# Optimization experiments

Hardware: AMD Instinct MI355X
Metric: run time of the kernel (lower is better)

Reference implementation:

```python
import jax, jax.numpy as jnp
import numpy as np

T, B, IN, H, E = 1024, 64, 64, 512, 128


def _gru_layer(x, Wih, Whh, bih, bhh):
    # x: [T, B, D_in]; Wih: [3H, D_in]; Whh: [3H, H]; PyTorch gate order: r, z, n
    gx = jnp.einsum('tbi,gi->tbg', x, Wih) + bih  # [T, B, 3H]

    def step(h, gx_t):
        gh = h @ Whh.T + bhh
        xr, xz, xn = jnp.split(gx_t, 3, axis=-1)
        hr, hz, hn = jnp.split(gh, 3, axis=-1)
        r = jax.nn.sigmoid(xr + hr)
        z = jax.nn.sigmoid(xz + hz)
        n = jnp.tanh(xn + r * hn)
        h_new = (1.0 - z) * n + z * h
        return h_new, h_new

    h0 = jnp.zeros((x.shape[1], Whh.shape[1]), x.dtype)
    _, ys = jax.lax.scan(step, h0, gx)
    return ys  # [T, B, H]


def setup_inputs() -> dict:
    key = jax.random.key(0)
    ks = iter(jax.random.split(key, 32))
    s = 0.05
    d = {'x': jax.random.normal(next(ks), (T, B, IN), jnp.float32)}
    # encoder GRU: layer0 IN->H, layer1 H->H; linear H->E
    d['e_Wih0'] = jax.random.normal(next(ks), (3 * H, IN), jnp.float32) * s
    d['e_Whh0'] = jax.random.normal(next(ks), (3 * H, H), jnp.float32) * s
    d['e_bih0'] = jax.random.normal(next(ks), (3 * H,), jnp.float32) * s
    d['e_bhh0'] = jax.random.normal(next(ks), (3 * H,), jnp.float32) * s
    d['e_Wih1'] = jax.random.normal(next(ks), (3 * H, H), jnp.float32) * s
    d['e_Whh1'] = jax.random.normal(next(ks), (3 * H, H), jnp.float32) * s
    d['e_bih1'] = jax.random.normal(next(ks), (3 * H,), jnp.float32) * s
    d['e_bhh1'] = jax.random.normal(next(ks), (3 * H,), jnp.float32) * s
    d['e_lW'] = jax.random.normal(next(ks), (E, H), jnp.float32) * s
    d['e_lb'] = jax.random.normal(next(ks), (E,), jnp.float32) * s
    # decoder GRU: layer0 E->H, layer1 H->H; linear H->IN
    d['d_Wih0'] = jax.random.normal(next(ks), (3 * H, E), jnp.float32) * s
    d['d_Whh0'] = jax.random.normal(next(ks), (3 * H, H), jnp.float32) * s
    d['d_bih0'] = jax.random.normal(next(ks), (3 * H,), jnp.float32) * s
    d['d_bhh0'] = jax.random.normal(next(ks), (3 * H,), jnp.float32) * s
    d['d_Wih1'] = jax.random.normal(next(ks), (3 * H, H), jnp.float32) * s
    d['d_Whh1'] = jax.random.normal(next(ks), (3 * H, H), jnp.float32) * s
    d['d_bih1'] = jax.random.normal(next(ks), (3 * H,), jnp.float32) * s
    d['d_bhh1'] = jax.random.normal(next(ks), (3 * H,), jnp.float32) * s
    d['d_lW'] = jax.random.normal(next(ks), (IN, H), jnp.float32) * s
    d['d_lb'] = jax.random.normal(next(ks), (IN,), jnp.float32) * s
    return d


def reference(x, e_Wih0, e_Whh0, e_bih0, e_bhh0, e_Wih1, e_Whh1, e_bih1, e_bhh1, e_lW, e_lb,
              d_Wih0, d_Whh0, d_bih0, d_bhh0, d_Wih1, d_Whh1, d_bih1, d_bhh1, d_lW, d_lb):
    # encoder
    h = _gru_layer(x, e_Wih0, e_Whh0, e_bih0, e_bhh0)
    h = _gru_layer(h, e_Wih1, e_Whh1, e_bih1, e_bhh1)
    z = jnp.einsum('tbh,eh->tbe', h, e_lW) + e_lb  # [T, B, E]
    # repeat last timestep embedding across time
    z_rep = jnp.broadcast_to(z[-1][None], (x.shape[0],) + z.shape[1:])
    # decoder
    g = _gru_layer(z_rep, d_Wih0, d_Whh0, d_bih0, d_bhh0)
    g = _gru_layer(g, d_Wih1, d_Whh1, d_bih1, d_bhh1)
    out = jnp.einsum('tbh,ih->tbi', g, d_lW) + d_lb  # [T, B, IN]
    return out
```

## Files before the change

kernel.cpp:

```cpp
#include <hip/hip_runtime.h>


#define SC_AGT __HIP_MEMORY_SCOPE_AGENT

typedef _Float16 half8 __attribute__((ext_vector_type(8)));
typedef float floatx4 __attribute__((ext_vector_type(4)));

union H8 { unsigned long long q[2]; half8 h; uint4 u4; };
union HU { _Float16 f; unsigned short u; };

static constexpr size_t OFF_FLAGS = 0;
static constexpr size_t OFF_GEP   = 16384;
static constexpr size_t OFF_Z     = 16448;
static constexpr size_t OFF_GXC   = OFF_Z + 64 * 128 * 4;
static constexpr size_t OFF_H0    = OFF_GXC + 64 * 1536 * 4;
static constexpr size_t OFF_H1    = OFF_H0 + 2 * 64 * 512 * 2;
static constexpr size_t OFF_G0    = OFF_H1 + 2 * 64 * 512 * 2;
static constexpr size_t OFF_G1    = OFF_G0 + 2 * 64 * 512 * 2;
static constexpr size_t OFF_LWP   = OFF_G1 + 2 * 64 * 512 * 2;
static constexpr size_t OFF_WF    = OFF_LWP + 64 * 512 * 2;

static constexpr int E_PREP    = 1;
static constexpr int E_ENC_BEG = 2;
static constexpr int E_ENC_END = 1026;
static constexpr int E_Z       = 1027;
static constexpr int E_GXC     = 1028;
static constexpr int E_DEC_BEG = 1029;
static constexpr int E_LAST    = 2054;

__device__ __forceinline__ unsigned long long ald64(const void* p) {
  return __hip_atomic_load((const unsigned long long*)p, __ATOMIC_RELAXED, SC_AGT);
}
__device__ __forceinline__ int ald32(const int* p) {
  return __hip_atomic_load(p, __ATOMIC_RELAXED, SC_AGT);
}
__device__ __forceinline__ void ast16(void* p, unsigned short v) {
  __hip_atomic_store((unsigned short*)p, v, __ATOMIC_RELAXED, SC_AGT);
}
__device__ __forceinline__ void ast32u(void* p, unsigned int v) {
  __hip_atomic_store((unsigned int*)p, v, __ATOMIC_RELAXED, SC_AGT);
}
__device__ __forceinline__ void astf(float* p, float v) {
  __hip_atomic_store(p, v, __ATOMIC_RELAXED, SC_AGT);
}

__device__ __forceinline__ float sigm(float x) { return 1.f / (1.f + __expf(-x)); }
__device__ __forceinline__ float tanh_f(float x) {
  x = fminf(fmaxf(x, -30.f), 30.f);
  const float e2 = __expf(2.f * x);
  return (e2 - 1.f) / (e2 + 1.f);
}

#define MFMA(a, b, c) __builtin_amdgcn_mfma_f32_16x16x32_f16((a), (b), (c), 0, 0, 0)

__device__ __forceinline__ void pollwait(const int* flags, int target) {
  const int lane = threadIdx.x & 63;
  for (;;) {
    const int v0 = ald32(flags + (size_t)lane * 16);
    const int v1 = ald32(flags + (size_t)(64 + lane) * 16);
    const int v2 = ald32(flags + (size_t)(128 + lane) * 16);
    const int v3 = ald32(flags + (size_t)(192 + lane) * 16);
    const bool ok = (v0 >= target) && (v1 >= target) && (v2 >= target) &&
                    (v3 >= target);
    if (__ballot(ok) == ~0ull) break;
    __builtin_amdgcn_s_sleep(2);
  }
  asm volatile("" ::: "memory");
}

__device__ __forceinline__ void pollwait_gep(const int* gep, int target) {
  for (;;) {
    if (ald32(gep) >= target) break;
    __builtin_amdgcn_s_sleep(1);
  }
  asm volatile("" ::: "memory");
}

__device__ __forceinline__ void tick_partials(
    const char* __restrict__ wf,
    int g0u, int g1u, int g2u, int g3u,
    int nk0, int nk1, int nk2, int nk3,
    int kc0, int kccnt, int hsplit,
    const float* __restrict__ xs,
    const _Float16* __restrict__ ax,
    const _Float16* __restrict__ ah,
    bool hvalid, int hcb, int lane,
    float* __restrict__ partsW) {
  const int quad = lane >> 4;
  H8 A[8];
#pragma unroll
  for (int c = 0; c < 8; ++c) {
    A[c].q[0] = 0ull;
    A[c].q[1] = 0ull;
    if (c < kccnt) {
      const int kc = kc0 + c;
      if (kc < hsplit) {
        if (xs) {
          const float* p = xs + kc * 32 + quad * 8;
          const float4 f0 = *(const float4*)p;
          const float4 f1 = *(const float4*)(p + 4);
          H8 t;
          t.h[0] = (_Float16)f0.x; t.h[1] = (_Float16)f0.y;
          t.h[2] = (_Float16)f0.z; t.h[3] = (_Float16)f0.w;
          t.h[4] = (_Float16)f1.x; t.h[5] = (_Float16)f1.y;
          t.h[6] = (_Float16)f1.z; t.h[7] = (_Float16)f1.w;
          A[c] = t;
        } else {
          const _Float16* p = ax + kc * 32 + quad * 8;
          A[c].q[0] = ald64(p);
          A[c].q[1] = ald64(p + 4);
        }
      } else if (hvalid) {
        const _Float16* p = ah + (kc - hsplit) * 32 + quad * 8;
        A[c].q[0] = ald64(p);
        A[c].q[1] = ald64(p + 4);
      }
    }
  }
  floatx4 ar = {0.f, 0.f, 0.f, 0.f};
  floatx4 az = ar, axn = ar, ahn = ar;
  const size_t lb = (size_t)lane * 16;
#pragma unroll
  for (int c = 0; c < 8; ++c) {
    if (c < kccnt) {
      const int kc = kc0 + c;
      const bool inH = (kc >= hsplit);
      if (!inH || hvalid) {
        {
          const char* b = wf + (size_t)(g0u + hcb * nk0 + kc) * 2048 + lb;
          H8 whi;
          whi.u4 = *(const uint4*)b;
          ar = MFMA(A[c].h, whi.h, ar);
        }
        {
          const char* b = wf + (size_t)(g1u + hcb * nk1 + kc) * 2048 + lb;
          H8 whi;
          whi.u4 = *(const uint4*)b;
          az = MFMA(A[c].h, whi.h, az);
        }
        if (!inH) {
          const char* b = wf + (size_t)(g2u + hcb * nk2 + kc) * 2048 + lb;
          H8 whi;
          whi.u4 = *(const uint4*)b;
          axn = MFMA(A[c].h, whi.h, axn);
        } else {
          const char* b = wf + (size_t)(g3u + hcb * nk3 + (kc - hsplit)) * 2048 + lb;
          H8 whi;
          whi.u4 = *(const uint4*)b;
          ahn = MFMA(A[c].h, whi.h, ahn);
        }
      }
    }
  }
  const int m = lane & 15;
#pragma unroll
  for (int i = 0; i < 4; ++i) {
    const int idx = (quad * 4 + i) * 16 + m;
    partsW[0 * 256 + idx] = ar[i];
    partsW[1 * 256 + idx] = az[i];
    partsW[2 * 256 + idx] = axn[i];
    partsW[3 * 256 + idx] = ahn[i];
  }
}

extern "C" __global__ void __launch_bounds__(256, 1) gru_ae_kernel(
    const float* __restrict__ x,
    const float* __restrict__ eW0i, const float* __restrict__ eW0h,
    const float* __restrict__ eb0i, const float* __restrict__ eb0h,
    const float* __restrict__ eW1i, const float* __restrict__ eW1h,
    const float* __restrict__ eb1i, const float* __restrict__ eb1h,
    const float* __restrict__ elW, const float* __restrict__ elb,
    const float* __restrict__ dW0i, const float* __restrict__ dW0h,
    const float* __restrict__ db0i, const float* __restrict__ db0h,
    const float* __restrict__ dW1i, const float* __restrict__ dW1h,
    const float* __restrict__ db1i, const float* __restrict__ db1h,
    const float* __restrict__ dlW, const float* __restrict__ dlb,
    float* __restrict__ out, char* __restrict__ ws) {
  const int tid = threadIdx.x, bid = blockIdx.x;
  const int lane = tid & 63, w = tid >> 6;
  const int quad = lane >> 4, m = lane & 15;
  const bool isP0 = bid < 128;
  const int pb = isP0 ? bid : bid - 128;
  const int rb = pb >> 5, hcb = pb & 31;

  int* flags = (int*)(ws + OFF_FLAGS);
  int* gep = (int*)(ws + OFF_GEP);
  float* zbuf = (float*)(ws + OFF_Z);
  float* gxc = (float*)(ws + OFF_GXC);
  _Float16* h0r = (_Float16*)(ws + OFF_H0);
  _Float16* h1r = (_Float16*)(ws + OFF_H1);
  _Float16* g0r = (_Float16*)(ws + OFF_G0);
  _Float16* g1r = (_Float16*)(ws + OFF_G1);
  _Float16* lWp = (_Float16*)(ws + OFF_LWP);
  const char* wfb = ws + OFF_WF;
  const char* wf0 = wfb;
  const char* wf1 = wfb + (size_t)1728 * 2048;
  const char* wf2 = wfb + (size_t)(1728 + 3072) * 2048;
  const char* wf3 = wfb + (size_t)(1728 + 3072 + 1536) * 2048;

  __shared__ float parts[4][4][256];
  __shared__ float outp[4][64];

  float hold_s = 0.f;
  float br = 0.f, bz = 0.f, bx = 0.f, bh = 0.f;
  float gxr_s = 0.f, gxz_s = 0.f, gxn_s = 0.f;

  for (int e = E_PREP; e <= E_LAST; ++e) {
    if (e > E_PREP) {
      if (w == 0) {
        if (bid == 0) {
          pollwait(flags, e - 1);
          __hip_atomic_store(gep, e - 1, __ATOMIC_RELAXED, SC_AGT);
        } else {
          pollwait_gep(gep, e - 1);
        }
      }
      __syncthreads();
    }

    if (e == E_PREP) {
      const int uend[4] = {1728, 4800, 6336, 9408};
      const int gub_[4][4] = {{0, 576, 1152, 1216}, {0, 1024, 2048, 2560},
                              {0, 512, 1024, 1024}, {0, 1024, 2048, 2560}};
      const int nkc_[4][4] = {{18, 18, 2, 16}, {32, 32, 16, 16},
                              {16, 16, 0, 16}, {32, 32, 16, 16}};
      const size_t wbL[4] = {0, (size_t)1728 * 2048, (size_t)4800 * 2048,
                             (size_t)6336 * 2048};
      const int wgid = bid * 4 + w;
      for (int unit = wgid; unit < 9408; unit += 1024) {
        int L = 0, lu = unit;
        if (unit >= uend[2]) { L = 3; lu = unit - uend[2]; }
        else if (unit >= uend[1]) { L = 2; lu = unit - uend[1]; }
        else if (unit >= uend[0]) { L = 1; lu = unit - uend[0]; }
        int g;
        if (lu < gub_[L][1]) g = 0;
        else if (lu < gub_[L][2]) g = 1;
        else if (nkc_[L][2] > 0 && lu < gub_[L][3]) g = 2;
        else g = 3;
        const int r2 = lu - gub_[L][g];
        const int nk = nkc_[L][g];
        const int hcbp = r2 / nk, kcp = r2 % nk;
        const int colp = hcbp * 16 + m;
        const float *Wi, *Wh;
        int Din;
        if (L == 0)      { Wi = eW0i; Wh = eW0h; Din = 64; }
        else if (L == 1) { Wi = eW1i; Wh = eW1h; Din = 512; }
        else if (L == 2) { Wi = nullptr; Wh = dW0h; Din = 0; }
        else             { Wi = dW1i; Wh = dW1h; Din = 512; }
        char* ub = (char*)(ws + OFF_WF) + wbL[L] + (size_t)lu * 2048 + lane * 16;
#pragma unroll
        for (int jj = 0; jj < 4; ++jj) {
          unsigned int hiw = 0, low = 0;
#pragma unroll
          for (int j2 = 0; j2 < 2; ++j2) {
            const int j = jj * 2 + j2;
            const int k = kcp * 32 + quad * 8 + j;
            float wv;
            if (g <= 1) {
              if (Wi && k < Din) wv = Wi[(size_t)(g * 512 + colp) * Din + k];
              else wv = Wh[(size_t)(g * 512 + colp) * 512 + (k - (Wi ? Din : 0))];
            } else if (g == 2) {
              wv = Wi[(size_t)(1024 + colp) * Din + k];
            } else {
              wv = Wh[(size_t)(1024 + colp) * 512 + k];
            }
            HU hi, lo;
            hi.f = (_Float16)wv;
            lo.f = (_Float16)(wv - (float)hi.f);
            hiw |= ((unsigned int)hi.u) << (16 * j2);
            low |= ((unsigned int)lo.u) << (16 * j2);
          }
          ast32u(ub + jj * 4, hiw);
          ast32u(ub + 1024 + jj * 4, low);
        }
      }
      const int gid = bid * 256 + tid;
      if (gid < 32768) {
        HU cv;
        cv.f = (_Float16)dlW[gid];
        ast16(lWp + gid, cv.u);
      }
    } else if (e <= E_ENC_END) {
      const int u = e - E_ENC_BEG;
      if (e == E_ENC_BEG) {
        const int colg = hcb * 16 + m;
        if (isP0) {
          br = eb0i[colg] + eb0h[colg];
          bz = eb0i[512 + colg] + eb0h[512 + colg];
          bx = eb0i[1024 + colg];
          bh = eb0h[1024 + colg];
        } else {
          br = eb1i[colg] + eb1h[colg];
          bz = eb1i[512 + colg] + eb1h[512 + colg];
          bx = eb1i[1024 + colg];
          bh = eb1h[1024 + colg];
        }
        hold_s = 0.f;
      }
      if (isP0) {
        if (u <= 1023) {
          const int t = u;
          const float* xs = x + ((size_t)t * 64 + rb * 16 + m) * 64;
          const _Float16* ah = h0r + (size_t)((t - 1) & 1) * 32768 + (rb * 16 + m) * 512;
          const int kc0 = (w == 0) ? 0 : (w == 1) ? 5 : (w == 2) ? 10 : 14;
          const int cnt = (w < 2) ? 5 : 4;
          tick_partials(wf0, 0, 576, 1152, 1216, 18, 18, 2, 16, kc0, cnt, 2,
                        xs, nullptr, ah, t >= 1, hcb, lane, &parts[w][0][0]);
        }
      } else {
        if (u >= 1) {
          const int t = u - 1;
          const _Float16* ax = h0r + (size_t)(t & 1) * 32768 + (rb * 16 + m) * 512;
          const _Float16* ah = h1r + (size_t)((t - 1) & 1) * 32768 + (rb * 16 + m) * 512;
          tick_partials(wf1, 0, 1024, 2048, 2560, 32, 32, 16, 16, w * 8, 8, 16,
                        nullptr, ax, ah, t >= 1, hcb, lane, &parts[w][0][0]);
        }
      }
    } else if (e == E_Z) {
      const int b = bid >> 2, e0 = (bid & 3) * 32;
      float acc = 0.f;
      if (lane < 32) {
        const _Float16* hsrc = h1r + (size_t)1 * 32768 + b * 512;
        const float* lwrow = elW + (size_t)(e0 + lane) * 512;
        for (int ch = 0; ch < 16; ++ch) {
          const int k = w * 128 + ch * 8;
          H8 a;
          a.q[0] = ald64(hsrc + k);
          a.q[1] = ald64(hsrc + k + 4);
          const float4 l0 = *(const float4*)(lwrow + k);
          const float4 l1 = *(const float4*)(lwrow + k + 4);
          acc += (float)a.h[0] * l0.x + (float)a.h[1] * l0.y +
                 (float)a.h[2] * l0.z + (float)a.h[3] * l0.w +
                 (float)a.h[4] * l1.x + (float)a.h[5] * l1.y +
                 (float)a.h[6] * l1.z + (float)a.h[7] * l1.w;
        }
      }
      outp[w][lane] = acc;
    } else if (e == E_GXC) {
      const int b = bid & 63, cb = (bid >> 6) * 384;
      for (int idx = w * 64 + lane; idx < 384; idx += 256) {
        const int c = cb + idx;
        float acc = db0i[c];
        const float* zr = zbuf + b * 128;
        const float* wr = dW0i + (size_t)c * 128;
        for (int k = 0; k < 128; ++k) acc += zr[k] * wr[k];
        astf(&gxc[(size_t)b * 1536 + c], acc);
      }
    } else {
      const int v = e - E_DEC_BEG;
      if (e == E_DEC_BEG) {
        const int colg = hcb * 16 + m;
        if (isP0) {
          br = db0h[colg];
          bz = db0h[512 + colg];
          bx = 0.f;
          bh = db0h[1024 + colg];
          const int row0 = rb * 16 + quad * 4 + w;
          gxr_s = gxc[(size_t)row0 * 1536 + colg];
          gxz_s = gxc[(size_t)row0 * 1536 + 512 + colg];
          gxn_s = gxc[(size_t)row0 * 1536 + 1024 + colg];
        } else {
          br = db1i[colg] + db1h[colg];
          bz = db1i[512 + colg] + db1h[512 + colg];
          bx = db1i[1024 + colg];
          bh = db1h[1024 + colg];
        }
        hold_s = 0.f;
      }
      if (isP0) {
        if (v <= 1023) {
          const int t = v;
          const _Float16* ah = g0r + (size_t)((t - 1) & 1) * 32768 + (rb * 16 + m) * 512;
          tick_partials(wf2, 0, 512, 0, 1024, 16, 16, 0, 16, w * 4, 4, 0,
                        nullptr, nullptr, ah, t >= 1, hcb, lane, &parts[w][0][0]);
        }
        if (pb < 64 && v >= 2) {
          const int t2 = v - 2;
          const _Float16* gsrc = g1r + (size_t)(t2 & 1) * 32768 + pb * 512;
          const _Float16* lrow = lWp + (size_t)lane * 512;
          float acc = 0.f;
          for (int ch = 0; ch < 16; ++ch) {
            const int k = w * 128 + ch * 8;
            H8 a, lw;
            a.q[0] = ald64(gsrc + k);
            a.q[1] = ald64(gsrc + k + 4);
            lw.u4 = *(const uint4*)(lrow + k);
#pragma unroll
            for (int j = 0; j < 8; ++j) acc += (float)a.h[j] * (float)lw.h[j];
          }
          outp[w][lane] = acc;
        }
      } else {
        if (v >= 1 && v <= 1024) {
          const int t = v - 1;
          const _Float16* ax = g0r + (size_t)(t & 1) * 32768 + (rb * 16 + m) * 512;
          const _Float16* ah = g1r + (size_t)((t - 1) & 1) * 32768 + (rb * 16 + m) * 512;
          tick_partials(wf3, 0, 1024, 2048, 2560, 32, 32, 16, 16, w * 8, 8, 16,
                        nullptr, ax, ah, t >= 1, hcb, lane, &parts[w][0][0]);
        }
      }
    }

    __syncthreads();

    if (e >= E_ENC_BEG && e <= E_ENC_END) {
      const int u = e - E_ENC_BEG;
      const bool doep = isP0 ? (u <= 1023) : (u >= 1);
      if (doep) {
        const int idx = (quad * 4 + w) * 16 + m;
        const float sr = parts[0][0][idx] + parts[1][0][idx] +
                         parts[2][0][idx] + parts[3][0][idx];
        const float sz = parts[0][1][idx] + parts[1][1][idx] +
                         parts[2][1][idx] + parts[3][1][idx];
        const float sx = parts[0][2][idx] + parts[1][2][idx] +
                         parts[2][2][idx] + parts[3][2][idx];
        const float sh = parts[0][3][idx] + parts[1][3][idx] +
                         parts[2][3][idx] + parts[3][3][idx];
        const float r = sigm(sr + br);
        const float z = sigm(sz + bz);
        const float n = tanh_f(sx + bx + r * (sh + bh));
        const float hh = (1.f - z) * n + z * hold_s;
        hold_s = hh;
        _Float16* ring = isP0 ? (h0r + (size_t)(u & 1) * 32768)
                              : (h1r + (size_t)((u - 1) & 1) * 32768);
        HU cv;
        cv.f = (_Float16)hh;
        ast16(ring + (rb * 16 + quad * 4 + w) * 512 + hcb * 16 + m, cv.u);
      }
    } else if (e == E_Z) {
      if (w == 0 && lane < 32) {
        const int b = bid >> 2, e0 = (bid & 3) * 32;
        const float s = outp[0][lane] + outp[1][lane] + outp[2][lane] +
                        outp[3][lane] + elb[e0 + lane];
        astf(&zbuf[b * 128 + e0 + lane], s);
      }
    } else if (e >= E_DEC_BEG) {
      const int v = e - E_DEC_BEG;
      if (isP0) {
        if (v <= 1023) {
          const int idx = (quad * 4 + w) * 16 + m;
          const float sr = parts[0][0][idx] + parts[1][0][idx] +
                           parts[2][0][idx] + parts[3][0][idx];
          const float sz = parts[0][1][idx] + parts[1][1][idx] +
                           parts[2][1][idx] + parts[3][1][idx];
          const float sh = parts[0][3][idx] + parts[1][3][idx] +
                           parts[2][3][idx] + parts[3][3][idx];
          const float r = sigm(sr + gxr_s + br);
          const float z = sigm(sz + gxz_s + bz);
          const float n = tanh_f(gxn_s + r * (sh + bh));
          const float hh = (1.f - z) * n + z * hold_s;
          hold_s = hh;
          HU cv;
          cv.f = (_Float16)hh;
          ast16(g0r + (size_t)(v & 1) * 32768 +
                    (rb * 16 + quad * 4 + w) * 512 + hcb * 16 + m,
                cv.u);
        }
        if (w == 0 && pb < 64 && v >= 2) {
          const int t2 = v - 2;
          const float s = outp[0][lane] + outp[1][lane] + outp[2][lane] +
                          outp[3][lane] + dlb[lane];
          astf(&out[((size_t)t2 * 64 + pb) * 64 + lane], s);
        }
      } else {
        if (v >= 1 && v <= 1024) {
          const int idx = (quad * 4 + w) * 16 + m;
          const float sr = parts[0][0][idx] + parts[1][0][idx] +
                           parts[2][0][idx] + parts[3][0][idx];
          const float sz = parts[0][1][idx] + parts[1][1][idx] +
                           parts[2][1][idx] + parts[3][1][idx];
          const float sx = parts[0][2][idx] + parts[1][2][idx] +
                           parts[2][2][idx] + parts[3][2][idx];
          const float sh = parts[0][3][idx] + parts[1][3][idx] +
                           parts[2][3][idx] + parts[3][3][idx];
          const float r = sigm(sr + br);
          const float z = sigm(sz + bz);
          const float n = tanh_f(sx + bx + r * (sh + bh));
          const float hh = (1.f - z) * n + z * hold_s;
          hold_s = hh;
          HU cv;
          cv.f = (_Float16)hh;
          ast16(g1r + (size_t)((v - 1) & 1) * 32768 +
                    (rb * 16 + quad * 4 + w) * 512 + hcb * 16 + m,
                cv.u);
        }
      }
    }

    __syncthreads();

    if (tid == 0) {
      __hip_atomic_store(&flags[bid * 16], e, __ATOMIC_RELAXED, SC_AGT);
    }
  }
}

extern "C" void kernel_launch(void* const* d_in, const int* in_sizes, int n_in,
                              void* d_out, int out_size, void* d_ws, size_t ws_size,
                              hipStream_t stream) {
  (void)in_sizes; (void)n_in; (void)out_size; (void)ws_size;
  hipMemsetAsync(d_ws, 0, 16448, stream);
  hipLaunchKernelGGL(gru_ae_kernel, dim3(256), dim3(256), 0, stream,
                     (const float*)d_in[0],
                     (const float*)d_in[1], (const float*)d_in[2],
                     (const float*)d_in[3], (const float*)d_in[4],
                     (const float*)d_in[5], (const float*)d_in[6],
                     (const float*)d_in[7], (const float*)d_in[8],
                     (const float*)d_in[9], (const float*)d_in[10],
                     (const float*)d_in[11], (const float*)d_in[12],
                     (const float*)d_in[13], (const float*)d_in[14],
                     (const float*)d_in[15], (const float*)d_in[16],
                     (const float*)d_in[17], (const float*)d_in[18],
                     (const float*)d_in[19], (const float*)d_in[20],
                     (float*)d_out, (char*)d_ws);
}
```

Baseline: 14.66 ms.

## Replace global per-step barrier with row-group flag waits and 4-deep rings

Per-timestep synchronization no longer waits on a global barrier coordinated by block 0. Each block now polls only the flags of the 64 blocks in its batch-row group across both layers, with a lagged target for producer-side blocks. The hidden-state rings grow from double to quadruple buffering so blocks can drift apart by a few steps without overwriting data still being read. The decoder output projection is reassigned to blocks inside each row group so its dependencies stay local. This removes the global barrier's serialization and latency, but relies on the ring depth and lag targets being correct to avoid races.

Result: slower. 16.03 ms (+9.4%).

```diff
diff --git a/kernel.cpp b/kernel.cpp
--- a/kernel.cpp
+++ b/kernel.cpp
@@ -13,11 +13,12 @@
 static constexpr size_t OFF_GEP   = 16384;
 static constexpr size_t OFF_Z     = 16448;
 static constexpr size_t OFF_GXC   = OFF_Z + 64 * 128 * 4;
+static constexpr size_t RING_SZ   = 4 * 64 * 512 * 2;
 static constexpr size_t OFF_H0    = OFF_GXC + 64 * 1536 * 4;
-static constexpr size_t OFF_H1    = OFF_H0 + 2 * 64 * 512 * 2;
-static constexpr size_t OFF_G0    = OFF_H1 + 2 * 64 * 512 * 2;
-static constexpr size_t OFF_G1    = OFF_G0 + 2 * 64 * 512 * 2;
-static constexpr size_t OFF_LWP   = OFF_G1 + 2 * 64 * 512 * 2;
+static constexpr size_t OFF_H1    = OFF_H0 + RING_SZ;
+static constexpr size_t OFF_G0    = OFF_H1 + RING_SZ;
+static constexpr size_t OFF_G1    = OFF_G0 + RING_SZ;
+static constexpr size_t OFF_LWP   = OFF_G1 + RING_SZ;
 static constexpr size_t OFF_WF    = OFF_LWP + 64 * 512 * 2;
 
 static constexpr int E_PREP    = 1;
@@ -72,6 +73,19 @@
   for (;;) {
     if (ald32(gep) >= target) break;
     __builtin_amdgcn_s_sleep(1);
+  }
+  asm volatile("" ::: "memory");
+}
+
+__device__ __forceinline__ void pollwait_grp2(const int* flags, int rb,
+                                              int tS0, int tS1) {
+  const int lane = threadIdx.x & 63;
+  const int b = (lane < 32) ? (rb * 32 + lane) : (128 + rb * 32 + (lane - 32));
+  const int tgt = (lane < 32) ? tS0 : tS1;
+  const int* p = flags + (size_t)b * 16;
+  for (;;) {
+    if (__ballot(ald32(p) >= tgt) == ~0ull) break;
+    __builtin_amdgcn_s_sleep(2);
   }
   asm volatile("" ::: "memory");
 }
@@ -182,6 +196,8 @@
   const bool isP0 = bid < 128;
   const int pb = isP0 ? bid : bid - 128;
   const int rb = pb >> 5, hcb = pb & 31;
+  const bool fl_own = isP0 && ((pb & 31) < 16);
+  const int fb = rb * 16 + (pb & 15);
 
   int* flags = (int*)(ws + OFF_FLAGS);
   int* gep = (int*)(ws + OFF_GEP);
@@ -208,11 +224,24 @@
   for (int e = E_PREP; e <= E_LAST; ++e) {
     if (e > E_PREP) {
       if (w == 0) {
-        if (bid == 0) {
-          pollwait(flags, e - 1);
-          __hip_atomic_store(gep, e - 1, __ATOMIC_RELAXED, SC_AGT);
+        const bool full = (e == E_ENC_BEG) || (e == E_Z) || (e == E_GXC) ||
+                          (e == E_DEC_BEG);
+        if (full) {
+          if (bid == 0) {
+            pollwait(flags, e - 1);
+            __hip_atomic_store(gep, e - 1, __ATOMIC_RELAXED, SC_AGT);
+          } else {
+            pollwait_gep(gep, e - 1);
+          }
         } else {
-          pollwait_gep(gep, e - 1);
+          int tS1;
+          if (isP0) {
+            const bool fl = (e > E_DEC_BEG) && ((pb & 31) < 16);
+            tS1 = fl ? (e - 1) : (e - 3);
+          } else {
+            tS1 = e - 1;
+          }
+          pollwait_grp2(flags, rb, e - 1, tS1);
         }
       }
       __syncthreads();
@@ -301,7 +330,7 @@
         if (u <= 1023) {
           const int t = u;
           const float* xs = x + ((size_t)t * 64 + rb * 16 + m) * 64;
-          const _Float16* ah = h0r + (size_t)((t - 1) & 1) * 32768 + (rb * 16 + m) * 512;
+          const _Float16* ah = h0r + (size_t)((t - 1) & 3) * 32768 + (rb * 16 + m) * 512;
           const int kc0 = (w == 0) ? 0 : (w == 1) ? 5 : (w == 2) ? 10 : 14;
           const int cnt = (w < 2) ? 5 : 4;
           tick_partials(wf0, 0, 576, 1152, 1216, 18, 18, 2, 16, kc0, cnt, 2,
@@ -310,8 +339,8 @@
       } else {
         if (u >= 1) {
           const int t = u - 1;
-          const _Float16* ax = h0r + (size_t)(t & 1) * 32768 + (rb * 16 + m) * 512;
-          const _Float16* ah = h1r + (size_t)((t - 1) & 1) * 32768 + (rb * 16 + m) * 512;
+          const _Float16* ax = h0r + (size_t)(t & 3) * 32768 + (rb * 16 + m) * 512;
+          const _Float16* ah = h1r + (size_t)((t - 1) & 3) * 32768 + (rb * 16 + m) * 512;
           tick_partials(wf1, 0, 1024, 2048, 2560, 32, 32, 16, 16, w * 8, 8, 16,
                         nullptr, ax, ah, t >= 1, hcb, lane, &parts[w][0][0]);
         }
@@ -320,7 +349,7 @@
       const int b = bid >> 2, e0 = (bid & 3) * 32;
       float acc = 0.f;
       if (lane < 32) {
-        const _Float16* hsrc = h1r + (size_t)1 * 32768 + b * 512;
+        const _Float16* hsrc = h1r + (size_t)3 * 32768 + b * 512;
         const float* lwrow = elW + (size_t)(e0 + lane) * 512;
         for (int ch = 0; ch < 16; ++ch) {
           const int k = w * 128 + ch * 8;
@@ -370,13 +399,13 @@
       if (isP0) {
         if (v <= 1023) {
           const int t = v;
-          const _Float16* ah = g0r + (size_t)((t - 1) & 1) * 32768 + (rb * 16 + m) * 512;
+          const _Float16* ah = g0r + (size_t)((t - 1) & 3) * 32768 + (rb * 16 + m) * 512;
           tick_partials(wf2, 0, 512, 0, 1024, 16, 16, 0, 16, w * 4, 4, 0,
                         nullptr, nullptr, ah, t >= 1, hcb, lane, &parts[w][0][0]);
         }
-        if (pb < 64 && v >= 2) {
+        if (fl_own && v >= 2) {
           const int t2 = v - 2;
-          const _Float16* gsrc = g1r + (size_t)(t2 & 1) * 32768 + pb * 512;
+          const _Float16* gsrc = g1r + (size_t)(t2 & 3) * 32768 + fb * 512;
           const _Float16* lrow = lWp + (size_t)lane * 512;
           float acc = 0.f;
           for (int ch = 0; ch < 16; ++ch) {
@@ -393,8 +422,8 @@
       } else {
         if (v >= 1 && v <= 1024) {
           const int t = v - 1;
-          const _Float16* ax = g0r + (size_t)(t & 1) * 32768 + (rb * 16 + m) * 512;
-          const _Float16* ah = g1r + (size_t)((t - 1) & 1) * 32768 + (rb * 16 + m) * 512;
+          const _Float16* ax = g0r + (size_t)(t & 3) * 32768 + (rb * 16 + m) * 512;
+          const _Float16* ah = g1r + (size_t)((t - 1) & 3) * 32768 + (rb * 16 + m) * 512;
           tick_partials(wf3, 0, 1024, 2048, 2560, 32, 32, 16, 16, w * 8, 8, 16,
                         nullptr, ax, ah, t >= 1, hcb, lane, &parts[w][0][0]);
         }
@@ -421,8 +450,8 @@
         const float n = tanh_f(sx + bx + r * (sh + bh));
         const float hh = (1.f - z) * n + z * hold_s;
         hold_s = hh;
-        _Float16* ring = isP0 ? (h0r + (size_t)(u & 1) * 32768)
-                              : (h1r + (size_t)((u - 1) & 1) * 32768);
+        _Float16* ring = isP0 ? (h0r + (size_t)(u & 3) * 32768)
+                              : (h1r + (size_t)((u - 1) & 3) * 32768);
         HU cv;
         cv.f = (_Float16)hh;
         ast16(ring + (rb * 16 + quad * 4 + w) * 512 + hcb * 16 + m, cv.u);
@@ -452,15 +481,15 @@
           hold_s = hh;
           HU cv;
           cv.f = (_Float16)hh;
-          ast16(g0r + (size_t)(v & 1) * 32768 +
+          ast16(g0r + (size_t)(v & 3) * 32768 +
                     (rb * 16 + quad * 4 + w) * 512 + hcb * 16 + m,
                 cv.u);
         }
-        if (w == 0 && pb < 64 && v >= 2) {
+        if (w == 0 && fl_own && v >= 2) {
           const int t2 = v - 2;
           const float s = outp[0][lane] + outp[1][lane] + outp[2][lane] +
                           outp[3][lane] + dlb[lane];
-          astf(&out[((size_t)t2 * 64 + pb) * 64 + lane], s);
+          astf(&out[((size_t)t2 * 64 + fb) * 64 + lane], s);
         }
       } else {
         if (v >= 1 && v <= 1024) {
@@ -480,7 +509,7 @@
           hold_s = hh;
           HU cv;
           cv.f = (_Float16)hh;
-          ast16(g1r + (size_t)((v - 1) & 1) * 32768 +
+          ast16(g1r + (size_t)((v - 1) & 3) * 32768 +
                     (rb * 16 + quad * 4 + w) * 512 + hcb * 16 + m,
                 cv.u);
         }
```
